# Kernel optimization log

Measured on AMD Instinct MI355X. Metric: run time of the kernel, lower is better.

Reference implementation:

```python
import jax, jax.numpy as jnp
import numpy as np

HEAD_DIM = 256
HIDDEN = 1536
INTERMEDIATE = 6144
NUM_KV_HEADS = 1
NUM_Q_HEADS = 8
SCALE = HEAD_DIM ** (-0.5)
PAST_LEN = 8191


def setup_inputs() -> dict:
    key = jax.random.key(0)
    ks = jax.random.split(key, 20)
    def lin(ki, fan_in, fan_out):
        # torch nn.Linear init: U(-1/sqrt(fan_in), 1/sqrt(fan_in)); stored (in, out) for x @ W
        bound = 1.0 / np.sqrt(fan_in)
        W = jax.random.uniform(ki, (fan_in, fan_out), jnp.float32, -bound, bound)
        b = jax.random.uniform(jax.random.fold_in(ki, 1), (fan_out,), jnp.float32, -bound, bound)
        return W, b
    Wq, bq = lin(ks[0], HIDDEN, NUM_Q_HEADS * HEAD_DIM)
    Wk, bk = lin(ks[1], HIDDEN, NUM_KV_HEADS * HEAD_DIM)
    Wv, bv = lin(ks[2], HIDDEN, NUM_KV_HEADS * HEAD_DIM)
    Wo, bo = lin(ks[3], NUM_Q_HEADS * HEAD_DIM, HIDDEN)
    Wg, bg = lin(ks[4], HIDDEN, INTERMEDIATE)
    Wu, bu = lin(ks[5], HIDDEN, INTERMEDIATE)
    Wd, bd = lin(ks[6], INTERMEDIATE, HIDDEN)
    x = jax.random.normal(ks[7], (1, 1, HIDDEN), jnp.float32)
    k_past = jax.random.normal(ks[8], (1, NUM_KV_HEADS, PAST_LEN, HEAD_DIM), jnp.float32)
    v_past = jax.random.normal(ks[9], (1, NUM_KV_HEADS, PAST_LEN, HEAD_DIM), jnp.float32)
    return dict(x=x, k_past=k_past, v_past=v_past,
                Wq=Wq, bq=bq, Wk=Wk, bk=bk, Wv=Wv, bv=bv, Wo=Wo, bo=bo,
                Wg=Wg, bg=bg, Wu=Wu, bu=bu, Wd=Wd, bd=bd)


def reference(x, k_past, v_past, Wq, bq, Wk, bk, Wv, bv, Wo, bo, Wg, bg, Wu, bu, Wd, bd):
    residual = x
    # projections; q: (1, Hq, 1, D), k/v: (1, Hkv, 1, D)
    q = (x @ Wq + bq).reshape(1, 1, NUM_Q_HEADS, HEAD_DIM).transpose(0, 2, 1, 3)
    k = (x @ Wk + bk).reshape(1, 1, NUM_KV_HEADS, HEAD_DIM).transpose(0, 2, 1, 3)
    v = (x @ Wv + bv).reshape(1, 1, NUM_KV_HEADS, HEAD_DIM).transpose(0, 2, 1, 3)
    k_full = jnp.concatenate([k_past, k], axis=2)  # (1, Hkv, S, D)
    v_full = jnp.concatenate([v_past, v], axis=2)
    # GQA: broadcast the single KV head across 8 Q heads (no materialized repeat)
    scores = jnp.einsum('bhqd,bksd->bhqs', q, k_full) * SCALE  # (1, Hq, 1, S)
    attn = jax.nn.softmax(scores, axis=-1)
    out = jnp.einsum('bhqs,bksd->bhqd', attn, v_full)  # (1, Hq, 1, D)
    out = out.transpose(0, 2, 1, 3).reshape(1, 1, NUM_Q_HEADS * HEAD_DIM)
    out = out @ Wo + bo
    x = residual + out
    # MLP: GELU(gate) * up -> down (exact erf GELU, matching torch nn.GELU default)
    ffn = (jax.nn.gelu(x @ Wg + bg, approximate=False) * (x @ Wu + bu)) @ Wd + bd
    return x + ffn
```

## Files before the change

kernel.cpp:

```cpp
#include <hip/hip_runtime.h>
#include <hip/hip_bf16.h>
#include <math.h>

#define PAST 8191
#define SCALEF 0.0625f

using bf = __hip_bfloat16;

__device__ __forceinline__ float bf2f(unsigned short u) {
    return __uint_as_float(((unsigned)u) << 16);
}
__device__ __forceinline__ void unpack8(uint4 r, float* f) {
    f[0] = __uint_as_float(r.x << 16);
    f[1] = __uint_as_float(r.x & 0xffff0000u);
    f[2] = __uint_as_float(r.y << 16);
    f[3] = __uint_as_float(r.y & 0xffff0000u);
    f[4] = __uint_as_float(r.z << 16);
    f[5] = __uint_as_float(r.z & 0xffff0000u);
    f[6] = __uint_as_float(r.w << 16);
    f[7] = __uint_as_float(r.w & 0xffff0000u);
}

template<bool BF16>
__device__ __forceinline__ void load8(const void* W, size_t off, float* f) {
    if constexpr (BF16) {
        uint4 r = *reinterpret_cast<const uint4*>((const unsigned short*)W + off);
        unpack8(r, f);
    } else {
        const float* p = (const float*)W + off;
        float4 a = *reinterpret_cast<const float4*>(p);
        float4 b = *reinterpret_cast<const float4*>(p + 4);
        f[0]=a.x; f[1]=a.y; f[2]=a.z; f[3]=a.w;
        f[4]=b.x; f[5]=b.y; f[6]=b.z; f[7]=b.w;
    }
}
template<bool BF16>
__device__ __forceinline__ void load4(const void* P, size_t off, float* f) {
    if constexpr (BF16) {
        uint2 r = *reinterpret_cast<const uint2*>((const unsigned short*)P + off);
        f[0] = __uint_as_float(r.x << 16); f[1] = __uint_as_float(r.x & 0xffff0000u);
        f[2] = __uint_as_float(r.y << 16); f[3] = __uint_as_float(r.y & 0xffff0000u);
    } else {
        float4 a = *reinterpret_cast<const float4*>((const float*)P + off);
        f[0]=a.x; f[1]=a.y; f[2]=a.z; f[3]=a.w;
    }
}
template<bool BF16>
__device__ __forceinline__ float load1(const void* P, int i) {
    if constexpr (BF16) return bf2f(((const unsigned short*)P)[i]);
    else return ((const float*)P)[i];
}

__global__ __launch_bounds__(256) void probe_kernel(const unsigned int* __restrict__ xw,
                                                    float* __restrict__ zws,
                                                    int* __restrict__ flag) {
    int idx = blockIdx.x * 256 + threadIdx.x;
    for (int k = idx; k < 38400; k += 10240) zws[k] = 0.f;
    if (blockIdx.x == 0) {
        __shared__ int cnt;
        if (threadIdx.x == 0) cnt = 0;
        __syncthreads();
        int ok = 0;
        for (int i = threadIdx.x; i < 768; i += 256) {
            unsigned e = (xw[i] >> 7) & 0xff;
            if (e >= 96 && e <= 142) ok++;
        }
        atomicAdd(&cnt, ok);
        __syncthreads();
        if (threadIdx.x == 0) *flag = (cnt > 500) ? 1 : 0;
    }
}

template<bool BF16>
__device__ __forceinline__ void gemv_rows16(const void* __restrict__ W, int ldw,
                                            const float* __restrict__ xs_wave,
                                            int row0, int j, float acc[8]) {
    #pragma unroll
    for (int i = 0; i < 16; i += 8) {
        float f[8][8];
        #pragma unroll
        for (int r = 0; r < 8; ++r)
            load8<BF16>(W, (size_t)(row0 + i + r) * ldw + j, f[r]);
        #pragma unroll
        for (int r = 0; r < 8; ++r) {
            float xv = xs_wave[i + r];
            #pragma unroll
            for (int q = 0; q < 8; ++q) acc[q] = fmaf(xv, f[r][q], acc[q]);
        }
    }
}

__device__ __forceinline__ void block_reduce_512(float acc[8], float* red,
                                                 int wave, int lane) {
    if (wave > 0) {
        float* dst = red + (wave - 1) * 512 + lane * 8;
        #pragma unroll
        for (int q = 0; q < 8; ++q) dst[q] = acc[q];
    }
    __syncthreads();
    if (wave == 0) {
        int o = lane * 8;
        #pragma unroll
        for (int q = 0; q < 8; ++q)
            acc[q] += red[o + q] + red[512 + o + q] + red[1024 + o + q];
    }
}

template<bool BF16>
__device__ void qkv_body(const void* __restrict__ x, const void* __restrict__ Wq,
                         const void* __restrict__ bq, const void* __restrict__ Wk,
                         const void* __restrict__ bk, const void* __restrict__ Wv,
                         const void* __restrict__ bv, float* __restrict__ qkv) {
    __shared__ float xs[64];
    __shared__ float red[3 * 512];
    int tid = threadIdx.x, wave = tid >> 6, lane = tid & 63;
    int i0 = blockIdx.y * 64;
    if (tid < 64) xs[tid] = load1<BF16>(x, i0 + tid);
    __syncthreads();
    int j = blockIdx.x * 512 + lane * 8;
    const void* W; const void* bias; int ldw, jl;
    if (j < 2048)      { W = Wq; bias = bq; ldw = 2048; jl = j; }
    else if (j < 2304) { W = Wk; bias = bk; ldw = 256;  jl = j - 2048; }
    else               { W = Wv; bias = bv; ldw = 256;  jl = j - 2304; }
    float acc[8] = {0,0,0,0,0,0,0,0};
    gemv_rows16<BF16>(W, ldw, xs + wave * 16, i0 + wave * 16, jl, acc);
    block_reduce_512(acc, red, wave, lane);
    if (wave == 0) {
        if (blockIdx.y == 0) {
            #pragma unroll
            for (int q = 0; q < 8; ++q) acc[q] += load1<BF16>(bias, jl + q);
        }
        float* out = qkv + (blockIdx.y & 1) * 2560;
        #pragma unroll
        for (int q = 0; q < 8; ++q) atomicAdd(&out[j + q], acc[q]);
    }
}
__global__ __launch_bounds__(256) void qkv_kernel(
    const void* x, const void* Wq, const void* bq, const void* Wk, const void* bk,
    const void* Wv, const void* bv, float* qkv, const int* flag) {
    if (*flag) qkv_body<true>(x, Wq, bq, Wk, bk, Wv, bv, qkv);
    else       qkv_body<false>(x, Wq, bq, Wk, bk, Wv, bv, qkv);
}

template<bool BF16>
__device__ void attn_body(const float* __restrict__ qkv, const void* __restrict__ k_past,
                          const void* __restrict__ v_past, float* __restrict__ attnout,
                          float* __restrict__ lpart) {
    __shared__ float wsum[8];
    __shared__ float red[3 * 2048];
    int tid = threadIdx.x, wave = tid >> 6, lane = tid & 63;
    if (tid < 8) wsum[tid] = 0.f;
    int d0 = lane * 4;
    const float* qkv1 = qkv + 2560;
    float4 qreg[8];
    #pragma unroll
    for (int h = 0; h < 8; ++h) {
        float4 a = *reinterpret_cast<const float4*>(qkv + h * 256 + d0);
        float4 b = *reinterpret_cast<const float4*>(qkv1 + h * 256 + d0);
        qreg[h].x = a.x + b.x; qreg[h].y = a.y + b.y;
        qreg[h].z = a.z + b.z; qreg[h].w = a.w + b.w;
    }
    float4 ka = *reinterpret_cast<const float4*>(qkv + 2048 + d0);
    float4 kb = *reinterpret_cast<const float4*>(qkv1 + 2048 + d0);
    float4 va = *reinterpret_cast<const float4*>(qkv + 2304 + d0);
    float4 vb = *reinterpret_cast<const float4*>(qkv1 + 2304 + d0);
    float knew[4] = {ka.x+kb.x, ka.y+kb.y, ka.z+kb.z, ka.w+kb.w};
    float vnew[4] = {va.x+vb.x, va.y+vb.y, va.z+vb.z, va.w+vb.w};
    __syncthreads();

    float o[8][4];
    #pragma unroll
    for (int h = 0; h < 8; ++h)
        #pragma unroll
        for (int r = 0; r < 4; ++r) o[h][r] = 0.f;
    float wl[8] = {0,0,0,0,0,0,0,0};

    int p0 = blockIdx.x * 64 + wave * 16;
    for (int it = 0; it < 16; it += 8) {
        float kf[8][4], vf[8][4];
        if (p0 + it + 7 < PAST) {
            #pragma unroll
            for (int r = 0; r < 8; ++r)
                load4<BF16>(k_past, (size_t)(p0 + it + r) * 256 + d0, kf[r]);
            #pragma unroll
            for (int r = 0; r < 8; ++r)
                load4<BF16>(v_past, (size_t)(p0 + it + r) * 256 + d0, vf[r]);
        } else {
            #pragma unroll
            for (int r = 0; r < 8; ++r) {
                int p = p0 + it + r;
                if (p < PAST) {
                    load4<BF16>(k_past, (size_t)p * 256 + d0, kf[r]);
                    load4<BF16>(v_past, (size_t)p * 256 + d0, vf[r]);
                } else {
                    kf[r][0]=knew[0]; kf[r][1]=knew[1]; kf[r][2]=knew[2]; kf[r][3]=knew[3];
                    vf[r][0]=vnew[0]; vf[r][1]=vnew[1]; vf[r][2]=vnew[2]; vf[r][3]=vnew[3];
                }
            }
        }
        float part[8][8];
        #pragma unroll
        for (int r = 0; r < 8; ++r)
            #pragma unroll
            for (int h = 0; h < 8; ++h)
                part[r][h] = qreg[h].x*kf[r][0] + qreg[h].y*kf[r][1]
                           + qreg[h].z*kf[r][2] + qreg[h].w*kf[r][3];
        #pragma unroll
        for (int m = 1; m < 64; m <<= 1) {
            #pragma unroll
            for (int r = 0; r < 8; ++r)
                #pragma unroll
                for (int h = 0; h < 8; ++h)
                    part[r][h] += __shfl_xor(part[r][h], m, 64);
        }
        #pragma unroll
        for (int r = 0; r < 8; ++r)
            #pragma unroll
            for (int h = 0; h < 8; ++h) {
                float w = expf(part[r][h] * SCALEF);
                wl[h] += w;
                #pragma unroll
                for (int rr = 0; rr < 4; ++rr) o[h][rr] = fmaf(w, vf[r][rr], o[h][rr]);
            }
    }
    if (lane == 0) {
        #pragma unroll
        for (int h = 0; h < 8; ++h) atomicAdd(&wsum[h], wl[h]);
    }
    if (wave > 0) {
        float* dst = red + (wave - 1) * 2048;
        #pragma unroll
        for (int h = 0; h < 8; ++h)
            #pragma unroll
            for (int r = 0; r < 4; ++r) dst[h * 256 + d0 + r] = o[h][r];
    }
    __syncthreads();
    if (wave == 0) {
        #pragma unroll
        for (int h = 0; h < 8; ++h)
            #pragma unroll
            for (int r = 0; r < 4; ++r) {
                float v = o[h][r] + red[h*256 + d0 + r] + red[2048 + h*256 + d0 + r]
                        + red[4096 + h*256 + d0 + r];
                atomicAdd(&attnout[h * 256 + d0 + r], v);
            }
    }
    if (tid < 8) atomicAdd(&lpart[tid * 64 + (blockIdx.x & 63)], wsum[tid]);
}
__global__ __launch_bounds__(256) void attn_kernel(
    const float* qkv, const void* k_past, const void* v_past, float* attnout,
    float* lpart, const int* flag) {
    if (*flag) attn_body<true>(qkv, k_past, v_past, attnout, lpart);
    else       attn_body<false>(qkv, k_past, v_past, attnout, lpart);
}

template<bool BF16>
__device__ void oproj_body(const float* __restrict__ attnout, const float* __restrict__ lpart,
                           const void* __restrict__ Wo, const void* __restrict__ bo,
                           const void* __restrict__ xin, float* __restrict__ x2) {
    __shared__ float xs[64];
    __shared__ float red[3 * 512];
    int tid = threadIdx.x, wave = tid >> 6, lane = tid & 63;
    int i0 = blockIdx.y * 64;
    int h = i0 >> 8;
    if (tid < 64) {
        float v = lpart[h * 64 + tid];
        #pragma unroll
        for (int m = 1; m < 64; m <<= 1) v += __shfl_xor(v, m, 64);
        xs[tid] = attnout[i0 + tid] * (1.0f / v);
    }
    __syncthreads();
    int j = blockIdx.x * 512 + lane * 8;
    float acc[8] = {0,0,0,0,0,0,0,0};
    gemv_rows16<BF16>(Wo, 1536, xs + wave * 16, i0 + wave * 16, j, acc);
    block_reduce_512(acc, red, wave, lane);
    if (wave == 0) {
        if (blockIdx.y == 0) {
            #pragma unroll
            for (int q = 0; q < 8; ++q)
                acc[q] += load1<BF16>(bo, j + q) + load1<BF16>(xin, j + q);
        }
        float* out = x2 + (blockIdx.y & 1) * 1536;
        #pragma unroll
        for (int q = 0; q < 8; ++q) atomicAdd(&out[j + q], acc[q]);
    }
}
__global__ __launch_bounds__(256) void oproj_kernel(
    const float* attnout, const float* lpart, const void* Wo, const void* bo,
    const void* xin, float* x2, const int* flag) {
    if (*flag) oproj_body<true>(attnout, lpart, Wo, bo, xin, x2);
    else       oproj_body<false>(attnout, lpart, Wo, bo, xin, x2);
}

template<bool BF16>
__device__ void gateup_body(const float* __restrict__ x2, const void* __restrict__ Wg,
                            const void* __restrict__ Wu, float* __restrict__ gacc,
                            float* __restrict__ uacc) {
    __shared__ float xs[64];
    __shared__ float red[3 * 512];
    int tid = threadIdx.x, wave = tid >> 6, lane = tid & 63;
    int i0 = blockIdx.y * 64;
    if (tid < 64) xs[tid] = x2[i0 + tid] + x2[1536 + i0 + tid];
    __syncthreads();
    const void* W = blockIdx.z ? Wu : Wg;
    float* out = (blockIdx.z ? uacc : gacc) + (blockIdx.y & 1) * 6144;
    int j = blockIdx.x * 512 + lane * 8;
    float acc[8] = {0,0,0,0,0,0,0,0};
    gemv_rows16<BF16>(W, 6144, xs + wave * 16, i0 + wave * 16, j, acc);
    block_reduce_512(acc, red, wave, lane);
    if (wave == 0) {
        #pragma unroll
        for (int q = 0; q < 8; ++q) atomicAdd(&out[j + q], acc[q]);
    }
}
__global__ __launch_bounds__(256) void gateup_kernel(
    const float* x2, const void* Wg, const void* Wu, float* gacc, float* uacc,
    const int* flag) {
    if (*flag) gateup_body<true>(x2, Wg, Wu, gacc, uacc);
    else       gateup_body<false>(x2, Wg, Wu, gacc, uacc);
}

template<bool BF16>
__device__ void down_body(const float* __restrict__ gacc, const float* __restrict__ uacc,
                          const void* __restrict__ bg, const void* __restrict__ bu,
                          const void* __restrict__ Wd, float* __restrict__ yacc) {
    __shared__ float xs[64];
    __shared__ float red[3 * 512];
    int tid = threadIdx.x, wave = tid >> 6, lane = tid & 63;
    int i0 = blockIdx.y * 64;
    if (tid < 64) {
        int i = i0 + tid;
        float g = gacc[i] + gacc[6144 + i] + load1<BF16>(bg, i);
        float u = uacc[i] + uacc[6144 + i] + load1<BF16>(bu, i);
        float ge = 0.5f * g * (1.0f + erff(g * 0.70710678118654752f));
        xs[tid] = ge * u;
    }
    __syncthreads();
    int j = blockIdx.x * 512 + lane * 8;
    float acc[8] = {0,0,0,0,0,0,0,0};
    gemv_rows16<BF16>(Wd, 1536, xs + wave * 16, i0 + wave * 16, j, acc);
    block_reduce_512(acc, red, wave, lane);
    if (wave == 0) {
        float* out = yacc + (blockIdx.y & 1) * 1536;
        #pragma unroll
        for (int q = 0; q < 8; ++q) atomicAdd(&out[j + q], acc[q]);
    }
}
__global__ __launch_bounds__(256) void down_kernel(
    const float* gacc, const float* uacc, const void* bg, const void* bu,
    const void* Wd, float* yacc, const int* flag) {
    if (*flag) down_body<true>(gacc, uacc, bg, bu, Wd, yacc);
    else       down_body<false>(gacc, uacc, bg, bu, Wd, yacc);
}

__global__ __launch_bounds__(256) void final_kernel(
    const float* __restrict__ x2, const float* __restrict__ yacc,
    const void* __restrict__ bd, void* __restrict__ out, const int* __restrict__ flag) {
    int j = blockIdx.x * 256 + threadIdx.x;
    if (j < 1536) {
        int isbf = *flag;
        float b = isbf ? bf2f(((const unsigned short*)bd)[j]) : ((const float*)bd)[j];
        float v = x2[j] + x2[1536 + j] + yacc[j] + yacc[1536 + j] + b;
        if (isbf) ((bf*)out)[j] = __float2bfloat16(v);
        else      ((float*)out)[j] = v;
    }
}

extern "C" void kernel_launch(void* const* d_in, const int* in_sizes, int n_in,
                              void* d_out, int out_size, void* d_ws, size_t ws_size,
                              hipStream_t stream) {
    const void* x  = d_in[0];
    const void* kp = d_in[1];
    const void* vp = d_in[2];
    const void* Wq = d_in[3];
    const void* bq = d_in[4];
    const void* Wk = d_in[5];
    const void* bk = d_in[6];
    const void* Wv = d_in[7];
    const void* bv = d_in[8];
    const void* Wo = d_in[9];
    const void* bo = d_in[10];
    const void* Wg = d_in[11];
    const void* bg = d_in[12];
    const void* Wu = d_in[13];
    const void* bu = d_in[14];
    const void* Wd = d_in[15];
    const void* bd = d_in[16];

    float* ws      = (float*)d_ws;
    float* qkv     = ws;
    float* x2      = ws + 5120;
    float* gacc    = ws + 8192;
    float* uacc    = ws + 20480;
    float* yacc    = ws + 32768;
    float* attnout = ws + 35840;
    float* lpart   = ws + 37888;
    int*  flag     = (int*)(ws + 40960);

    probe_kernel<<<40, 256, 0, stream>>>((const unsigned int*)x, ws, flag);

    qkv_kernel<<<dim3(5, 24), 256, 0, stream>>>(x, Wq, bq, Wk, bk, Wv, bv, qkv, flag);
    attn_kernel<<<128, 256, 0, stream>>>(qkv, kp, vp, attnout, lpart, flag);
    oproj_kernel<<<dim3(3, 32), 256, 0, stream>>>(attnout, lpart, Wo, bo, x, x2, flag);
    gateup_kernel<<<dim3(12, 24, 2), 256, 0, stream>>>(x2, Wg, Wu, gacc, uacc, flag);
    down_kernel<<<dim3(3, 96), 256, 0, stream>>>(gacc, uacc, bg, bu, Wd, yacc, flag);
    final_kernel<<<6, 256, 0, stream>>>(x2, yacc, bd, d_out, flag);
}
```

Measured before the change: 262.1 us.

## Fuse all decoder stages into one persistent kernel with grid barriers

```diff
diff --git a/kernel.cpp b/kernel.cpp
--- a/kernel.cpp
+++ b/kernel.cpp
@@ -4,6 +4,7 @@
 
 #define PAST 8191
 #define SCALEF 0.0625f
+#define NB 256u
 
 using bf = __hip_bfloat16;
 
@@ -51,26 +52,33 @@
     else return ((const float*)P)[i];
 }
 
-__global__ __launch_bounds__(256) void probe_kernel(const unsigned int* __restrict__ xw,
-                                                    float* __restrict__ zws,
-                                                    int* __restrict__ flag) {
-    int idx = blockIdx.x * 256 + threadIdx.x;
-    for (int k = idx; k < 38400; k += 10240) zws[k] = 0.f;
-    if (blockIdx.x == 0) {
-        __shared__ int cnt;
-        if (threadIdx.x == 0) cnt = 0;
-        __syncthreads();
-        int ok = 0;
-        for (int i = threadIdx.x; i < 768; i += 256) {
-            unsigned e = (xw[i] >> 7) & 0xff;
-            if (e >= 96 && e <= 142) ok++;
-        }
-        atomicAdd(&cnt, ok);
-        __syncthreads();
-        if (threadIdx.x == 0) *flag = (cnt > 500) ? 1 : 0;
-    }
-}
-
+__device__ __forceinline__ void gbar(unsigned* cnt, unsigned target) {
+    __syncthreads();
+    if (threadIdx.x == 0) {
+        __threadfence();
+        atomicAdd(cnt, 1u);
+        while (__hip_atomic_load(cnt, __ATOMIC_ACQUIRE, __HIP_MEMORY_SCOPE_AGENT) < target)
+            __builtin_amdgcn_s_sleep(2);
+        __threadfence();
+    }
+    __syncthreads();
+}
+
+template<bool BF16>
+__device__ __forceinline__ void gemv_rows8(const void* __restrict__ W, int ldw,
+                                           const float* __restrict__ xs_wave,
+                                           int row0, int j, float acc[8]) {
+    float f[8][8];
+    #pragma unroll
+    for (int r = 0; r < 8; ++r)
+        load8<BF16>(W, (size_t)(row0 + r) * ldw + j, f[r]);
+    #pragma unroll
+    for (int r = 0; r < 8; ++r) {
+        float xv = xs_wave[r];
+        #pragma unroll
+        for (int q = 0; q < 8; ++q) acc[q] = fmaf(xv, f[r][q], acc[q]);
+    }
+}
 template<bool BF16>
 __device__ __forceinline__ void gemv_rows16(const void* __restrict__ W, int ldw,
                                             const float* __restrict__ xs_wave,
@@ -106,92 +114,92 @@
     }
 }
 
-template<bool BF16>
-__device__ void qkv_body(const void* __restrict__ x, const void* __restrict__ Wq,
-                         const void* __restrict__ bq, const void* __restrict__ Wk,
-                         const void* __restrict__ bk, const void* __restrict__ Wv,
-                         const void* __restrict__ bv, float* __restrict__ qkv) {
-    __shared__ float xs[64];
-    __shared__ float red[3 * 512];
-    int tid = threadIdx.x, wave = tid >> 6, lane = tid & 63;
-    int i0 = blockIdx.y * 64;
-    if (tid < 64) xs[tid] = load1<BF16>(x, i0 + tid);
-    __syncthreads();
-    int j = blockIdx.x * 512 + lane * 8;
-    const void* W; const void* bias; int ldw, jl;
-    if (j < 2048)      { W = Wq; bias = bq; ldw = 2048; jl = j; }
-    else if (j < 2304) { W = Wk; bias = bk; ldw = 256;  jl = j - 2048; }
-    else               { W = Wv; bias = bv; ldw = 256;  jl = j - 2304; }
-    float acc[8] = {0,0,0,0,0,0,0,0};
-    gemv_rows16<BF16>(W, ldw, xs + wave * 16, i0 + wave * 16, jl, acc);
-    block_reduce_512(acc, red, wave, lane);
-    if (wave == 0) {
-        if (blockIdx.y == 0) {
-            #pragma unroll
-            for (int q = 0; q < 8; ++q) acc[q] += load1<BF16>(bias, jl + q);
-        }
-        float* out = qkv + (blockIdx.y & 1) * 2560;
-        #pragma unroll
-        for (int q = 0; q < 8; ++q) atomicAdd(&out[j + q], acc[q]);
-    }
-}
-__global__ __launch_bounds__(256) void qkv_kernel(
-    const void* x, const void* Wq, const void* bq, const void* Wk, const void* bk,
-    const void* Wv, const void* bv, float* qkv, const int* flag) {
-    if (*flag) qkv_body<true>(x, Wq, bq, Wk, bk, Wv, bv, qkv);
-    else       qkv_body<false>(x, Wq, bq, Wk, bk, Wv, bv, qkv);
-}
-
-template<bool BF16>
-__device__ void attn_body(const float* __restrict__ qkv, const void* __restrict__ k_past,
-                          const void* __restrict__ v_past, float* __restrict__ attnout,
-                          float* __restrict__ lpart) {
-    __shared__ float wsum[8];
-    __shared__ float red[3 * 2048];
-    int tid = threadIdx.x, wave = tid >> 6, lane = tid & 63;
-    if (tid < 8) wsum[tid] = 0.f;
-    int d0 = lane * 4;
-    const float* qkv1 = qkv + 2560;
-    float4 qreg[8];
-    #pragma unroll
-    for (int h = 0; h < 8; ++h) {
-        float4 a = *reinterpret_cast<const float4*>(qkv + h * 256 + d0);
-        float4 b = *reinterpret_cast<const float4*>(qkv1 + h * 256 + d0);
-        qreg[h].x = a.x + b.x; qreg[h].y = a.y + b.y;
-        qreg[h].z = a.z + b.z; qreg[h].w = a.w + b.w;
-    }
-    float4 ka = *reinterpret_cast<const float4*>(qkv + 2048 + d0);
-    float4 kb = *reinterpret_cast<const float4*>(qkv1 + 2048 + d0);
-    float4 va = *reinterpret_cast<const float4*>(qkv + 2304 + d0);
-    float4 vb = *reinterpret_cast<const float4*>(qkv1 + 2304 + d0);
-    float knew[4] = {ka.x+kb.x, ka.y+kb.y, ka.z+kb.z, ka.w+kb.w};
-    float vnew[4] = {va.x+vb.x, va.y+vb.y, va.z+vb.z, va.w+vb.w};
-    __syncthreads();
-
-    float o[8][4];
-    #pragma unroll
-    for (int h = 0; h < 8; ++h)
-        #pragma unroll
-        for (int r = 0; r < 4; ++r) o[h][r] = 0.f;
-    float wl[8] = {0,0,0,0,0,0,0,0};
-
-    int p0 = blockIdx.x * 64 + wave * 16;
-    for (int it = 0; it < 16; it += 8) {
+
+template<bool BF16>
+__device__ void mega_body(const void* __restrict__ x, const void* __restrict__ kp,
+                          const void* __restrict__ vp,
+                          const void* __restrict__ Wq, const void* __restrict__ bq,
+                          const void* __restrict__ Wk, const void* __restrict__ bk,
+                          const void* __restrict__ Wv, const void* __restrict__ bv,
+                          const void* __restrict__ Wo, const void* __restrict__ bo,
+                          const void* __restrict__ Wg, const void* __restrict__ bg,
+                          const void* __restrict__ Wu, const void* __restrict__ bu,
+                          const void* __restrict__ Wd, const void* __restrict__ bd,
+                          void* __restrict__ out, float* __restrict__ ws,
+                          unsigned* __restrict__ bar,
+                          float* xs, float* red, float* wsum) {
+    const int bid = blockIdx.x;
+    const int tid = threadIdx.x, wave = tid >> 6, lane = tid & 63;
+
+    float* qkvA  = ws;
+    float* x2A   = ws + 5120;
+    float* gaccA = ws + 8192;
+    float* uaccA = ws + 20480;
+    float* yacc  = ws + 32768;
+    float* attnS = ws + 38912;
+    float* lpart = ws + 71680;
+
+    if (bid < 240) {
+        int jb = bid / 48, ib = bid % 48;
+        int i0 = ib * 32;
+        if (tid < 32) xs[tid] = load1<BF16>(x, i0 + tid);
+        __syncthreads();
+        int j = jb * 512 + lane * 8;
+        const void* W; const void* bias; int ldw, jl;
+        if (j < 2048)      { W = Wq; bias = bq; ldw = 2048; jl = j; }
+        else if (j < 2304) { W = Wk; bias = bk; ldw = 256;  jl = j - 2048; }
+        else               { W = Wv; bias = bv; ldw = 256;  jl = j - 2304; }
+        float acc[8] = {0,0,0,0,0,0,0,0};
+        gemv_rows8<BF16>(W, ldw, xs + wave * 8, i0 + wave * 8, jl, acc);
+        block_reduce_512(acc, red, wave, lane);
+        if (wave == 0) {
+            if (ib == 0) {
+                #pragma unroll
+                for (int q = 0; q < 8; ++q) acc[q] += load1<BF16>(bias, jl + q);
+            }
+            float* o = qkvA + (ib & 1) * 2560;
+            #pragma unroll
+            for (int q = 0; q < 8; ++q) atomicAdd(&o[j + q], acc[q]);
+        }
+    }
+    gbar(bar, 2 * NB);
+
+    {
+        if (tid < 8) wsum[tid] = 0.f;
+        __syncthreads();
+        int d0 = lane * 4;
+        const float* q1 = qkvA + 2560;
+        float4 qreg[8];
+        #pragma unroll
+        for (int h = 0; h < 8; ++h) {
+            float4 a = *reinterpret_cast<const float4*>(qkvA + h * 256 + d0);
+            float4 b = *reinterpret_cast<const float4*>(q1 + h * 256 + d0);
+            qreg[h].x = a.x + b.x; qreg[h].y = a.y + b.y;
+            qreg[h].z = a.z + b.z; qreg[h].w = a.w + b.w;
+        }
+        float4 ka = *reinterpret_cast<const float4*>(qkvA + 2048 + d0);
+        float4 kb = *reinterpret_cast<const float4*>(q1 + 2048 + d0);
+        float4 va = *reinterpret_cast<const float4*>(qkvA + 2304 + d0);
+        float4 vb2 = *reinterpret_cast<const float4*>(q1 + 2304 + d0);
+        float knew[4] = {ka.x+kb.x, ka.y+kb.y, ka.z+kb.z, ka.w+kb.w};
+        float vnew[4] = {va.x+vb2.x, va.y+vb2.y, va.z+vb2.z, va.w+vb2.w};
+
+        int p0 = bid * 32 + wave * 8;
         float kf[8][4], vf[8][4];
-        if (p0 + it + 7 < PAST) {
+        if (p0 + 7 < PAST) {
             #pragma unroll
             for (int r = 0; r < 8; ++r)
-                load4<BF16>(k_past, (size_t)(p0 + it + r) * 256 + d0, kf[r]);
+                load4<BF16>(kp, (size_t)(p0 + r) * 256 + d0, kf[r]);
             #pragma unroll
             for (int r = 0; r < 8; ++r)
-                load4<BF16>(v_past, (size_t)(p0 + it + r) * 256 + d0, vf[r]);
+                load4<BF16>(vp, (size_t)(p0 + r) * 256 + d0, vf[r]);
         } else {
             #pragma unroll
             for (int r = 0; r < 8; ++r) {
-                int p = p0 + it + r;
+                int p = p0 + r;
                 if (p < PAST) {
-                    load4<BF16>(k_past, (size_t)p * 256 + d0, kf[r]);
-                    load4<BF16>(v_past, (size_t)p * 256 + d0, vf[r]);
+                    load4<BF16>(kp, (size_t)p * 256 + d0, kf[r]);
+                    load4<BF16>(vp, (size_t)p * 256 + d0, vf[r]);
                 } else {
                     kf[r][0]=knew[0]; kf[r][1]=knew[1]; kf[r][2]=knew[2]; kf[r][3]=knew[3];
                     vf[r][0]=vnew[0]; vf[r][1]=vnew[1]; vf[r][2]=vnew[2]; vf[r][3]=vnew[3];
@@ -213,6 +221,12 @@
                 for (int h = 0; h < 8; ++h)
                     part[r][h] += __shfl_xor(part[r][h], m, 64);
         }
+        float o[8][4];
+        #pragma unroll
+        for (int h = 0; h < 8; ++h)
+            #pragma unroll
+            for (int r = 0; r < 4; ++r) o[h][r] = 0.f;
+        float wl[8] = {0,0,0,0,0,0,0,0};
         #pragma unroll
         for (int r = 0; r < 8; ++r)
             #pragma unroll
@@ -222,148 +236,149 @@
                 #pragma unroll
                 for (int rr = 0; rr < 4; ++rr) o[h][rr] = fmaf(w, vf[r][rr], o[h][rr]);
             }
-    }
-    if (lane == 0) {
-        #pragma unroll
-        for (int h = 0; h < 8; ++h) atomicAdd(&wsum[h], wl[h]);
-    }
-    if (wave > 0) {
-        float* dst = red + (wave - 1) * 2048;
-        #pragma unroll
-        for (int h = 0; h < 8; ++h)
-            #pragma unroll
-            for (int r = 0; r < 4; ++r) dst[h * 256 + d0 + r] = o[h][r];
-    }
+        if (lane == 0) {
+            #pragma unroll
+            for (int h = 0; h < 8; ++h) atomicAdd(&wsum[h], wl[h]);
+        }
+        if (wave > 0) {
+            float* dst = red + (wave - 1) * 2048;
+            #pragma unroll
+            for (int h = 0; h < 8; ++h)
+                #pragma unroll
+                for (int r = 0; r < 4; ++r) dst[h * 256 + d0 + r] = o[h][r];
+        }
+        __syncthreads();
+        if (wave == 0) {
+            float* os = attnS + (size_t)(bid & 15) * 2048;
+            #pragma unroll
+            for (int h = 0; h < 8; ++h)
+                #pragma unroll
+                for (int r = 0; r < 4; ++r) {
+                    float v = o[h][r] + red[h*256 + d0 + r] + red[2048 + h*256 + d0 + r]
+                            + red[4096 + h*256 + d0 + r];
+                    atomicAdd(&os[h * 256 + d0 + r], v);
+                }
+        }
+        if (tid < 8) atomicAdd(&lpart[tid * 64 + (bid & 63)], wsum[tid]);
+    }
+    gbar(bar, 3 * NB);
+
+    if (bid < 96) {
+        int jb = bid / 32, ib = bid % 32;
+        int i0 = ib * 64;
+        int h = i0 >> 8;
+        if (tid < 64) {
+            float v = lpart[h * 64 + tid];
+            #pragma unroll
+            for (int m = 1; m < 64; m <<= 1) v += __shfl_xor(v, m, 64);
+            int i = i0 + tid;
+            float s = 0.f;
+            #pragma unroll
+            for (int st = 0; st < 16; ++st) s += attnS[(size_t)st * 2048 + i];
+            xs[tid] = s * (1.0f / v);
+        }
+        __syncthreads();
+        int j = jb * 512 + lane * 8;
+        float acc[8] = {0,0,0,0,0,0,0,0};
+        gemv_rows16<BF16>(Wo, 1536, xs + wave * 16, i0 + wave * 16, j, acc);
+        block_reduce_512(acc, red, wave, lane);
+        if (wave == 0) {
+            if (ib == 0) {
+                #pragma unroll
+                for (int q = 0; q < 8; ++q)
+                    acc[q] += load1<BF16>(bo, j + q) + load1<BF16>(x, j + q);
+            }
+            float* o = x2A + (ib & 1) * 1536;
+            #pragma unroll
+            for (int q = 0; q < 8; ++q) atomicAdd(&o[j + q], acc[q]);
+        }
+    }
+    gbar(bar, 4 * NB);
+
+    for (int vb = bid; vb < 576; vb += 256) {
+        int z = vb / 288, r2 = vb % 288, jb = r2 % 12, ib = r2 / 12;
+        int i0 = ib * 64;
+        if (tid < 64) xs[tid] = x2A[i0 + tid] + x2A[1536 + i0 + tid];
+        __syncthreads();
+        const void* W = z ? Wu : Wg;
+        float* outp = (z ? uaccA : gaccA) + (ib & 1) * 6144;
+        int j = jb * 512 + lane * 8;
+        float acc[8] = {0,0,0,0,0,0,0,0};
+        gemv_rows16<BF16>(W, 6144, xs + wave * 16, i0 + wave * 16, j, acc);
+        block_reduce_512(acc, red, wave, lane);
+        if (wave == 0) {
+            #pragma unroll
+            for (int q = 0; q < 8; ++q) atomicAdd(&outp[j + q], acc[q]);
+        }
+        __syncthreads();
+    }
+    gbar(bar, 5 * NB);
+
+    for (int vb = bid; vb < 288; vb += 256) {
+        int jb = vb % 3, ib = vb / 3;
+        int i0 = ib * 64;
+        if (tid < 64) {
+            int i = i0 + tid;
+            float g = gaccA[i] + gaccA[6144 + i] + load1<BF16>(bg, i);
+            float u = uaccA[i] + uaccA[6144 + i] + load1<BF16>(bu, i);
+            float ge = 0.5f * g * (1.0f + erff(g * 0.70710678118654752f));
+            xs[tid] = ge * u;
+        }
+        __syncthreads();
+        int j = jb * 512 + lane * 8;
+        float acc[8] = {0,0,0,0,0,0,0,0};
+        gemv_rows16<BF16>(Wd, 1536, xs + wave * 16, i0 + wave * 16, j, acc);
+        block_reduce_512(acc, red, wave, lane);
+        if (wave == 0) {
+            float* o = yacc + (ib & 3) * 1536;
+            #pragma unroll
+            for (int q = 0; q < 8; ++q) atomicAdd(&o[j + q], acc[q]);
+        }
+        __syncthreads();
+    }
+    gbar(bar, 6 * NB);
+
+    if (bid == 0) {
+        for (int j = tid; j < 1536; j += 256) {
+            float b = load1<BF16>(bd, j);
+            float v = x2A[j] + x2A[1536 + j]
+                    + yacc[j] + yacc[1536 + j] + yacc[3072 + j] + yacc[4608 + j] + b;
+            if constexpr (BF16) ((bf*)out)[j] = __float2bfloat16(v);
+            else                ((float*)out)[j] = v;
+        }
+    }
+}
+
+__global__ __launch_bounds__(256, 2) void mega_kernel(
+    const void* x, const void* kp, const void* vp,
+    const void* Wq, const void* bq, const void* Wk, const void* bk,
+    const void* Wv, const void* bv, const void* Wo, const void* bo,
+    const void* Wg, const void* bg, const void* Wu, const void* bu,
+    const void* Wd, const void* bd, void* out, float* ws, unsigned* bar) {
+    __shared__ float xs[64];
+    __shared__ float red[3 * 2048];
+    __shared__ float wsum[8];
+    __shared__ int pcnt;
+    if (threadIdx.x == 0) pcnt = 0;
     __syncthreads();
-    if (wave == 0) {
-        #pragma unroll
-        for (int h = 0; h < 8; ++h)
-            #pragma unroll
-            for (int r = 0; r < 4; ++r) {
-                float v = o[h][r] + red[h*256 + d0 + r] + red[2048 + h*256 + d0 + r]
-                        + red[4096 + h*256 + d0 + r];
-                atomicAdd(&attnout[h * 256 + d0 + r], v);
-            }
-    }
-    if (tid < 8) atomicAdd(&lpart[tid * 64 + (blockIdx.x & 63)], wsum[tid]);
-}
-__global__ __launch_bounds__(256) void attn_kernel(
-    const float* qkv, const void* k_past, const void* v_past, float* attnout,
-    float* lpart, const int* flag) {
-    if (*flag) attn_body<true>(qkv, k_past, v_past, attnout, lpart);
-    else       attn_body<false>(qkv, k_past, v_past, attnout, lpart);
-}
-
-template<bool BF16>
-__device__ void oproj_body(const float* __restrict__ attnout, const float* __restrict__ lpart,
-                           const void* __restrict__ Wo, const void* __restrict__ bo,
-                           const void* __restrict__ xin, float* __restrict__ x2) {
-    __shared__ float xs[64];
-    __shared__ float red[3 * 512];
-    int tid = threadIdx.x, wave = tid >> 6, lane = tid & 63;
-    int i0 = blockIdx.y * 64;
-    int h = i0 >> 8;
-    if (tid < 64) {
-        float v = lpart[h * 64 + tid];
-        #pragma unroll
-        for (int m = 1; m < 64; m <<= 1) v += __shfl_xor(v, m, 64);
-        xs[tid] = attnout[i0 + tid] * (1.0f / v);
-    }
+    {
+        const unsigned* xw = (const unsigned*)x;
+        int ok = 0;
+        for (int i = threadIdx.x; i < 768; i += 256) {
+            unsigned e = (xw[i] >> 7) & 0xff;
+            if (e >= 96 && e <= 142) ok++;
+        }
+        atomicAdd(&pcnt, ok);
+    }
+    int idx = blockIdx.x * 256 + threadIdx.x;
+    for (int k = idx; k < 72192; k += 65536) ws[k] = 0.f;
     __syncthreads();
-    int j = blockIdx.x * 512 + lane * 8;
-    float acc[8] = {0,0,0,0,0,0,0,0};
-    gemv_rows16<BF16>(Wo, 1536, xs + wave * 16, i0 + wave * 16, j, acc);
-    block_reduce_512(acc, red, wave, lane);
-    if (wave == 0) {
-        if (blockIdx.y == 0) {
-            #pragma unroll
-            for (int q = 0; q < 8; ++q)
-                acc[q] += load1<BF16>(bo, j + q) + load1<BF16>(xin, j + q);
-        }
-        float* out = x2 + (blockIdx.y & 1) * 1536;
-        #pragma unroll
-        for (int q = 0; q < 8; ++q) atomicAdd(&out[j + q], acc[q]);
-    }
-}
-__global__ __launch_bounds__(256) void oproj_kernel(
-    const float* attnout, const float* lpart, const void* Wo, const void* bo,
-    const void* xin, float* x2, const int* flag) {
-    if (*flag) oproj_body<true>(attnout, lpart, Wo, bo, xin, x2);
-    else       oproj_body<false>(attnout, lpart, Wo, bo, xin, x2);
-}
-
-template<bool BF16>
-__device__ void gateup_body(const float* __restrict__ x2, const void* __restrict__ Wg,
-                            const void* __restrict__ Wu, float* __restrict__ gacc,
-                            float* __restrict__ uacc) {
-    __shared__ float xs[64];
-    __shared__ float red[3 * 512];
-    int tid = threadIdx.x, wave = tid >> 6, lane = tid & 63;
-    int i0 = blockIdx.y * 64;
-    if (tid < 64) xs[tid] = x2[i0 + tid] + x2[1536 + i0 + tid];
-    __syncthreads();
-    const void* W = blockIdx.z ? Wu : Wg;
-    float* out = (blockIdx.z ? uacc : gacc) + (blockIdx.y & 1) * 6144;
-    int j = blockIdx.x * 512 + lane * 8;
-    float acc[8] = {0,0,0,0,0,0,0,0};
-    gemv_rows16<BF16>(W, 6144, xs + wave * 16, i0 + wave * 16, j, acc);
-    block_reduce_512(acc, red, wave, lane);
-    if (wave == 0) {
-        #pragma unroll
-        for (int q = 0; q < 8; ++q) atomicAdd(&out[j + q], acc[q]);
-    }
-}
-__global__ __launch_bounds__(256) void gateup_kernel(
-    const float* x2, const void* Wg, const void* Wu, float* gacc, float* uacc,
-    const int* flag) {
-    if (*flag) gateup_body<true>(x2, Wg, Wu, gacc, uacc);
-    else       gateup_body<false>(x2, Wg, Wu, gacc, uacc);
-}
-
-template<bool BF16>
-__device__ void down_body(const float* __restrict__ gacc, const float* __restrict__ uacc,
-                          const void* __restrict__ bg, const void* __restrict__ bu,
-                          const void* __restrict__ Wd, float* __restrict__ yacc) {
-    __shared__ float xs[64];
-    __shared__ float red[3 * 512];
-    int tid = threadIdx.x, wave = tid >> 6, lane = tid & 63;
-    int i0 = blockIdx.y * 64;
-    if (tid < 64) {
-        int i = i0 + tid;
-        float g = gacc[i] + gacc[6144 + i] + load1<BF16>(bg, i);
-        float u = uacc[i] + uacc[6144 + i] + load1<BF16>(bu, i);
-        float ge = 0.5f * g * (1.0f + erff(g * 0.70710678118654752f));
-        xs[tid] = ge * u;
-    }
-    __syncthreads();
-    int j = blockIdx.x * 512 + lane * 8;
-    float acc[8] = {0,0,0,0,0,0,0,0};
-    gemv_rows16<BF16>(Wd, 1536, xs + wave * 16, i0 + wave * 16, j, acc);
-    block_reduce_512(acc, red, wave, lane);
-    if (wave == 0) {
-        float* out = yacc + (blockIdx.y & 1) * 1536;
-        #pragma unroll
-        for (int q = 0; q < 8; ++q) atomicAdd(&out[j + q], acc[q]);
-    }
-}
-__global__ __launch_bounds__(256) void down_kernel(
-    const float* gacc, const float* uacc, const void* bg, const void* bu,
-    const void* Wd, float* yacc, const int* flag) {
-    if (*flag) down_body<true>(gacc, uacc, bg, bu, Wd, yacc);
-    else       down_body<false>(gacc, uacc, bg, bu, Wd, yacc);
-}
-
-__global__ __launch_bounds__(256) void final_kernel(
-    const float* __restrict__ x2, const float* __restrict__ yacc,
-    const void* __restrict__ bd, void* __restrict__ out, const int* __restrict__ flag) {
-    int j = blockIdx.x * 256 + threadIdx.x;
-    if (j < 1536) {
-        int isbf = *flag;
-        float b = isbf ? bf2f(((const unsigned short*)bd)[j]) : ((const float*)bd)[j];
-        float v = x2[j] + x2[1536 + j] + yacc[j] + yacc[1536 + j] + b;
-        if (isbf) ((bf*)out)[j] = __float2bfloat16(v);
-        else      ((float*)out)[j] = v;
-    }
+    bool isbf = pcnt > 500;
+    gbar(bar, NB);
+    if (isbf) mega_body<true >(x, kp, vp, Wq, bq, Wk, bk, Wv, bv, Wo, bo,
+                               Wg, bg, Wu, bu, Wd, bd, out, ws, bar, xs, red, wsum);
+    else      mega_body<false>(x, kp, vp, Wq, bq, Wk, bk, Wv, bv, Wo, bo,
+                               Wg, bg, Wu, bu, Wd, bd, out, ws, bar, xs, red, wsum);
 }
 
 extern "C" void kernel_launch(void* const* d_in, const int* in_sizes, int n_in,
@@ -387,22 +402,11 @@
     const void* Wd = d_in[15];
     const void* bd = d_in[16];
 
-    float* ws      = (float*)d_ws;
-    float* qkv     = ws;
-    float* x2      = ws + 5120;
-    float* gacc    = ws + 8192;
-    float* uacc    = ws + 20480;
-    float* yacc    = ws + 32768;
-    float* attnout = ws + 35840;
-    float* lpart   = ws + 37888;
-    int*  flag     = (int*)(ws + 40960);
-
-    probe_kernel<<<40, 256, 0, stream>>>((const unsigned int*)x, ws, flag);
-
-    qkv_kernel<<<dim3(5, 24), 256, 0, stream>>>(x, Wq, bq, Wk, bk, Wv, bv, qkv, flag);
-    attn_kernel<<<128, 256, 0, stream>>>(qkv, kp, vp, attnout, lpart, flag);
-    oproj_kernel<<<dim3(3, 32), 256, 0, stream>>>(attnout, lpart, Wo, bo, x, x2, flag);
-    gateup_kernel<<<dim3(12, 24, 2), 256, 0, stream>>>(x2, Wg, Wu, gacc, uacc, flag);
-    down_kernel<<<dim3(3, 96), 256, 0, stream>>>(gacc, uacc, bg, bu, Wd, yacc, flag);
-    final_kernel<<<6, 256, 0, stream>>>(x2, yacc, bd, d_out, flag);
-}
+    float* ws = (float*)d_ws;
+    unsigned* bar = (unsigned*)(ws + 100000);
+
+    hipMemsetAsync(bar, 0, 64, stream);
+    mega_kernel<<<256, 256, 0, stream>>>(x, kp, vp, Wq, bq, Wk, bk, Wv, bv,
+                                         Wo, bo, Wg, bg, Wu, bu, Wd, bd,
+                                         d_out, ws, bar);
+}
```

After: 401.0 us. +53.0%, slower.
